# Kernel tuning notes

Measured on AMD Instinct MI355X. Metric: run time of the kernel, lower is better.

The kernel has to match this reference:

```python
import jax, jax.numpy as jnp
import numpy as np

EPS = float(np.finfo(np.float64).eps)  # np.finfo(float).eps as in the torch code
N_WAY = 64  # num_classes


def setup_inputs() -> dict:
    key = jax.random.key(0)
    k1, k2, k3, k4 = jax.random.split(key, 4)
    N, d, C, Ns = 4096, 256, N_WAY, 1024
    embeddings = jax.random.normal(k1, (N, d), dtype=jnp.float32)
    # per-node sigma from RelationNetwork; keep in [0.5, 1.5] so exp(-dist/2) is well-scaled
    sigma = jax.random.uniform(k2, (N, 1), dtype=jnp.float32, minval=0.5, maxval=1.5)
    alpha = jnp.full((1,), 0.99, dtype=jnp.float32)  # propagation coefficient
    support_labels = jax.random.randint(k3, (Ns,), 0, C)
    return {
        "embeddings": embeddings,
        "sigma": sigma,
        "alpha": alpha,
        "support_labels": support_labels,
        "alpha_k": 20,
    }


def reference(embeddings, sigma, alpha, support_labels, alpha_k):
    N, d = embeddings.shape
    C = N_WAY
    Ns = support_labels.shape[0]
    # embeddings divided by sigma twice, as in the original
    e = embeddings / (sigma + EPS)
    e = e / (sigma + EPS)
    # W_ij = mean_k (e_i - e_j)^2  via |a|^2 + |b|^2 - 2 a.b (same math, no NxNxd tensor)
    sq = jnp.sum(e * e, axis=1)  # [N]
    dist = (sq[:, None] + sq[None, :] - 2.0 * (e @ e.T)) / d  # [N, N]
    W = jnp.exp(-dist / 2.0)
    # topk per row -> scatter 1s -> symmetrize
    _, idx = jax.lax.top_k(W, alpha_k)  # [N, k]
    rows = jnp.arange(N)[:, None]
    mask = jnp.zeros_like(W).at[rows, idx].set(1.0)
    mask = ((mask + mask.T) > 0).astype(W.dtype)
    W = W * mask
    # symmetric degree normalization: S = D^-1/2 W D^-1/2
    D = W.sum(axis=0)
    d_inv_sqrt = jnp.sqrt(1.0 / (D + EPS))
    S = d_inv_sqrt[:, None] * W * d_inv_sqrt[None, :]
    # labels: one-hot support, zeros for queries
    one_hot_support = jax.nn.one_hot(support_labels, C, dtype=W.dtype)
    label_all = jnp.concatenate([one_hot_support, jnp.zeros((N - Ns, C), W.dtype)], axis=0)
    # closed-form propagation: F = (I - alpha*S + eps)^-1 @ label_all
    A = jnp.eye(N, dtype=W.dtype) - alpha[0] * S + EPS
    F = jnp.linalg.solve(A, label_all)  # same math as inverse @ labels
    return F
```

## Files before the change

### kernel.cpp

```cpp
#include <hip/hip_runtime.h>
#include <math.h>

#define NN 4096
#define DD 256
#define NCLS 64
#define EPSF 2.2204460492503131e-16f
#define NITER 36
#define KMAX 64
#define TASK 32
#define NNZ_CAP (NN * 2 * KMAX)
#define MAXTASK (NNZ_CAP / TASK)
#define LDP 40

typedef __attribute__((ext_vector_type(8))) _Float16 half8;
typedef __attribute__((ext_vector_type(4))) float f32x4;

__global__ void k_prep(const float* __restrict__ emb, const float* __restrict__ sig,
                       _Float16* __restrict__ ehi, _Float16* __restrict__ elo,
                       float* __restrict__ sq) {
  int row = blockIdx.x, t = threadIdx.x;
  float s = sig[row] + EPSF;
  float v = emb[row * DD + t];
  v = v / s; v = v / s;
  _Float16 h = (_Float16)v;
  _Float16 l = (_Float16)(v - (float)h);
  ehi[row * DD + t] = h;
  elo[row * DD + t] = l;
  __shared__ float red[DD];
  red[t] = v * v; __syncthreads();
  for (int off = 128; off > 0; off >>= 1) {
    if (t < off) red[t] += red[t + off];
    __syncthreads();
  }
  if (t == 0) sq[row] = red[0];
}

__global__ __launch_bounds__(256) void k_gemmw(
    const _Float16* __restrict__ ehi, const _Float16* __restrict__ elo,
    const float* __restrict__ sq, float* __restrict__ W) {
  __shared__ _Float16 Ah[128][LDP];
  __shared__ _Float16 Al[128][LDP];
  __shared__ _Float16 Bh[128][LDP];
  __shared__ _Float16 Bl[128][LDP];
  int t = threadIdx.x;
  int lane = t & 63, wv = t >> 6;
  int wm = wv >> 1, wn = wv & 1;
  int rowbase = blockIdx.y * 128, colbase = blockIdx.x * 128;
  f32x4 acc[4][4];
#pragma unroll
  for (int m = 0; m < 4; ++m)
#pragma unroll
    for (int n = 0; n < 4; ++n) acc[m][n] = (f32x4){0.f, 0.f, 0.f, 0.f};
  int fr = lane & 15, kc = (lane >> 4) * 8;
  for (int k0 = 0; k0 < DD; k0 += 32) {
    for (int q = t; q < 512; q += 256) {
      int lr = q >> 2, ls = (q & 3) * 8;
      size_t ga = (size_t)(rowbase + lr) * DD + k0 + ls;
      size_t gb = (size_t)(colbase + lr) * DD + k0 + ls;
      *(uint4*)&Ah[lr][ls] = *(const uint4*)&ehi[ga];
      *(uint4*)&Al[lr][ls] = *(const uint4*)&elo[ga];
      *(uint4*)&Bh[lr][ls] = *(const uint4*)&ehi[gb];
      *(uint4*)&Bl[lr][ls] = *(const uint4*)&elo[gb];
    }
    __syncthreads();
    half8 ah[4], al[4], bh[4], bl[4];
#pragma unroll
    for (int m = 0; m < 4; ++m) {
      ah[m] = *(const half8*)&Ah[wm * 64 + m * 16 + fr][kc];
      al[m] = *(const half8*)&Al[wm * 64 + m * 16 + fr][kc];
    }
#pragma unroll
    for (int n = 0; n < 4; ++n) {
      bh[n] = *(const half8*)&Bh[wn * 64 + n * 16 + fr][kc];
      bl[n] = *(const half8*)&Bl[wn * 64 + n * 16 + fr][kc];
    }
#pragma unroll
    for (int m = 0; m < 4; ++m)
#pragma unroll
      for (int n = 0; n < 4; ++n) {
        acc[m][n] = __builtin_amdgcn_mfma_f32_16x16x32_f16(ah[m], bh[n], acc[m][n], 0, 0, 0);
        acc[m][n] = __builtin_amdgcn_mfma_f32_16x16x32_f16(ah[m], bl[n], acc[m][n], 0, 0, 0);
        acc[m][n] = __builtin_amdgcn_mfma_f32_16x16x32_f16(al[m], bh[n], acc[m][n], 0, 0, 0);
      }
    __syncthreads();
  }
#pragma unroll
  for (int m = 0; m < 4; ++m) {
#pragma unroll
    for (int reg = 0; reg < 4; ++reg) {
      int i = rowbase + wm * 64 + m * 16 + (lane >> 4) * 4 + reg;
      float sqi = sq[i];
#pragma unroll
      for (int n = 0; n < 4; ++n) {
        int j = colbase + wn * 64 + n * 16 + (lane & 15);
        float dist = (sqi + sq[j] - 2.0f * acc[m][n][reg]) * (1.0f / DD);
        W[(size_t)i * NN + j] = expf(-0.5f * dist);
      }
    }
  }
}

__global__ void k_zero(unsigned* __restrict__ p, int n) {
  int i = blockIdx.x * blockDim.x + threadIdx.x;
  if (i < n) p[i] = 0u;
}

__global__ __launch_bounds__(256) void k_topk(const float* __restrict__ W,
                                              unsigned* __restrict__ mask,
                                              const int* __restrict__ kptr) {
  int row = blockIdx.x;
  int t = threadIdx.x, lane = t & 63, w = t >> 6;
  int K = kptr[0]; if (K > KMAX) K = KMAX;
  const float* Wr = &W[(size_t)row * NN];
  float val[16];
#pragma unroll
  for (int i = 0; i < 16; ++i) val[i] = Wr[w * 1024 + i * 64 + lane];
  unsigned rm = 0;
  __shared__ float lv[4][KMAX];
  __shared__ int   lc[4][KMAX];
  for (int k = 0; k < K; ++k) {
    float vb = -1e38f; int cb = 0x7fffffff;
#pragma unroll
    for (int i = 0; i < 16; ++i) {
      bool ok = !((rm >> i) & 1u);
      if (ok && val[i] > vb) { vb = val[i]; cb = w * 1024 + i * 64 + lane; }
    }
    for (int off = 32; off > 0; off >>= 1) {
      float ov = __shfl_xor(vb, off, 64);
      int   oc = __shfl_xor(cb, off, 64);
      if (ov > vb || (ov == vb && oc < cb)) { vb = ov; cb = oc; }
    }
    if ((cb & 63) == lane) { int i = (cb >> 6) & 15; rm |= 1u << i; }
    if (lane == 0) { lv[w][k] = vb; lc[w][k] = cb; }
  }
  __syncthreads();
  if (w == 0) {
    float cv[4]; int cc[4]; unsigned crm = 0;
#pragma unroll
    for (int j = 0; j < 4; ++j) {
      if (lane < K) { cv[j] = lv[j][lane]; cc[j] = lc[j][lane]; }
      else { cv[j] = -1e38f; cc[j] = 0x7fffffff; }
    }
    for (int k = 0; k < K; ++k) {
      float vb = -1e38f; int cb = 0x7fffffff;
#pragma unroll
      for (int j = 0; j < 4; ++j) {
        bool ok = !((crm >> j) & 1u);
        if (ok && (cv[j] > vb || (cv[j] == vb && cc[j] < cb))) { vb = cv[j]; cb = cc[j]; }
      }
      for (int off = 32; off > 0; off >>= 1) {
        float ov = __shfl_xor(vb, off, 64);
        int   oc = __shfl_xor(cb, off, 64);
        if (ov > vb || (ov == vb && oc < cb)) { vb = ov; cb = oc; }
      }
#pragma unroll
      for (int j = 0; j < 4; ++j) if (cc[j] == cb) crm |= 1u << j;
      if (lane == 0) {
        atomicOr(&mask[row * 128 + (cb >> 5)], 1u << (cb & 31));
        atomicOr(&mask[cb * 128 + (row >> 5)], 1u << (row & 31));
      }
    }
  }
}

__global__ void k_degree(const unsigned* __restrict__ mask, const float* __restrict__ W,
                         float* __restrict__ Dinv, int* __restrict__ deg) {
  int row = blockIdx.x, t = threadIdx.x;
  unsigned m = mask[row * 128 + t];
  float dsum = 0.f; int cnt = __popc(m);
  unsigned mm = m;
  while (mm) {
    int b = __ffs(mm) - 1; mm &= mm - 1;
    dsum += W[(size_t)row * NN + t * 32 + b];
  }
  __shared__ float rs[128];
  __shared__ int   rc[128];
  rs[t] = dsum; rc[t] = cnt; __syncthreads();
  for (int off = 64; off > 0; off >>= 1) {
    if (t < off) { rs[t] += rs[t + off]; rc[t] += rc[t + off]; }
    __syncthreads();
  }
  if (t == 0) { deg[row] = rc[0]; Dinv[row] = sqrtf(1.0f / (rs[0] + EPSF)); }
}

__global__ void k_scan(const int* __restrict__ deg, int* __restrict__ rowptr) {
  int t = threadIdx.x;
  int lane = t & 63, w = t >> 6;
  int loc[16]; int s = 0;
  for (int u = 0; u < 16; ++u) { loc[u] = s; s += deg[t * 16 + u]; }
  int tot = s, inc = s;
  for (int off = 1; off < 64; off <<= 1) {
    int n = __shfl_up(inc, off, 64);
    if (lane >= off) inc += n;
  }
  __shared__ int wt[4];
  if (lane == 63) wt[w] = inc;
  __syncthreads();
  int base = 0;
  for (int u = 0; u < w; ++u) base += wt[u];
  int excl = base + inc - tot;
  for (int u = 0; u < 16; ++u) rowptr[t * 16 + u] = excl + loc[u];
  if (t == 255) rowptr[NN] = excl + tot;
}

__global__ void k_fill(const unsigned* __restrict__ mask, const float* __restrict__ W,
                       const float* __restrict__ Dinv, const int* __restrict__ rowptr,
                       int2* __restrict__ cv, const float* __restrict__ alphap) {
  int row = blockIdx.x, t = threadIdx.x;
  float alpha = alphap[0];
  unsigned m = mask[row * 128 + t];
  __shared__ int wcnt[128];
  wcnt[t] = __popc(m); __syncthreads();
  int pre = 0;
  for (int u = 0; u < t; ++u) pre += wcnt[u];
  int base = rowptr[row] + pre;
  float di = Dinv[row];
  while (m) {
    int b = __ffs(m) - 1; m &= m - 1;
    int j = t * 32 + b;
    float v = alpha * W[(size_t)row * NN + j] * di * Dinv[j];
    cv[base] = make_int2(j, __float_as_int(v));
    ++base;
  }
}

__global__ void k_taskrow(const int* __restrict__ rowptr, int* __restrict__ taskrow) {
  int task = blockIdx.x * blockDim.x + threadIdx.x;
  int nnz = rowptr[NN];
  int ntask = (nnz + TASK - 1) / TASK;
  if (task >= ntask) return;
  int start = task * TASK;
  int lo = 0, hi = NN;
  while (hi - lo > 1) {
    int mid = (lo + hi) >> 1;
    if (rowptr[mid] <= start) lo = mid; else hi = mid;
  }
  taskrow[task] = lo;
}

__global__ __launch_bounds__(256) void k_init_state(
    const int* __restrict__ labels, int Ns, float* __restrict__ X,
    float* __restrict__ R, float* __restrict__ D0, float* __restrict__ SV) {
  int idx = blockIdx.x * 256 + threadIdx.x;
  int i = idx >> 6, c = idx & 63;
  float b = (i < Ns && labels[i] == c) ? 1.0f : 0.0f;
  X[idx] = 0.0f; R[idx] = b; D0[idx] = b; SV[idx] = 0.0f;
}

__global__ __launch_bounds__(256) void k_spmm(
    const int* __restrict__ rowptr, const int2* __restrict__ cv,
    const int* __restrict__ taskrow, const float* __restrict__ Dc,
    float* __restrict__ SV) {
  int lane = threadIdx.x & 63;
  int wave0 = (blockIdx.x * 256 + threadIdx.x) >> 6;
  int nwaves = (gridDim.x * 256) >> 6;
  int nnz = rowptr[NN];
  int ntask = (nnz + TASK - 1) / TASK;
  for (int task = wave0; task < ntask; task += nwaves) {
    int start = task * TASK;
    int end = start + TASK; if (end > nnz) end = nnz;
    float prod[TASK];
#pragma unroll
    for (int u = 0; u < TASK; ++u) {
      int p = start + u;
      if (p < end) {
        int2 c = cv[p];
        prod[u] = __int_as_float(c.y) * Dc[(size_t)c.x * 64 + lane];
      } else prod[u] = 0.0f;
    }
    int r = taskrow[task];
    int rend = rowptr[r + 1];
    float acc = 0.0f;
#pragma unroll
    for (int u = 0; u < TASK; ++u) {
      int p = start + u;
      if (p >= end) break;
      while (p >= rend) {
        atomicAdd(&SV[(size_t)r * 64 + lane], acc);
        acc = 0.0f; ++r; rend = rowptr[r + 1];
      }
      acc += prod[u];
    }
    atomicAdd(&SV[(size_t)r * 64 + lane], acc);
  }
}

__global__ __launch_bounds__(256) void k_update(
    float* __restrict__ X, float* __restrict__ R, const float* __restrict__ Dcur,
    float* __restrict__ Dnxt, float* __restrict__ SV,
    const float* __restrict__ alphap, int it) {
  int idx = (blockIdx.x * 256 + threadIdx.x) * 2;
  float alpha = alphap[0];
  float sigma1 = 1.0f / alpha;
  float rho_prev = alpha;
  for (int k = 0; k < it; ++k) rho_prev = 1.0f / (2.0f * sigma1 - rho_prev);
  float rho = 1.0f / (2.0f * sigma1 - rho_prev);
  float c1 = rho * rho_prev, c2 = 2.0f * rho / alpha;
  float2 s = *(float2*)&SV[idx];
  *(float2*)&SV[idx] = make_float2(0.f, 0.f);
  float2 d = *(const float2*)&Dcur[idx];
  float2 x = *(float2*)&X[idx];
  float2 r = *(float2*)&R[idx];
  x.x += d.x; x.y += d.y;
  r.x -= (d.x - s.x); r.y -= (d.y - s.y);
  float2 dn;
  dn.x = c1 * d.x + c2 * r.x; dn.y = c1 * d.y + c2 * r.y;
  *(float2*)&X[idx] = x;
  *(float2*)&R[idx] = r;
  *(float2*)&Dnxt[idx] = dn;
}

static inline char* carve(char*& p, size_t bytes) {
  char* r = p;
  size_t a = (bytes + 255) & ~(size_t)255;
  p += a;
  return r;
}

extern "C" void kernel_launch(void* const* d_in, const int* in_sizes, int n_in,
                              void* d_out, int out_size, void* d_ws, size_t ws_size,
                              hipStream_t stream) {
  const float* emb    = (const float*)d_in[0];
  const float* sigma  = (const float*)d_in[1];
  const float* alphap = (const float*)d_in[2];
  const int*   labels = (const int*)d_in[3];
  const int*   kptr   = (const int*)d_in[4];
  int Ns = in_sizes[3];
  float* X = (float*)d_out;

  char* p = (char*)d_ws;
  _Float16* ehi    = (_Float16*)carve(p, (size_t)NN * DD * 2);
  _Float16* elo    = (_Float16*)carve(p, (size_t)NN * DD * 2);
  float*    sq     = (float*)carve(p, NN * 4);
  float*    Wm     = (float*)carve(p, (size_t)NN * NN * 4);
  unsigned* mask   = (unsigned*)carve(p, NN * 128 * 4);
  float*    Dinv   = (float*)carve(p, NN * 4);
  int*      deg    = (int*)carve(p, NN * 4);
  int*      rowptr = (int*)carve(p, (NN + 1) * 4);
  int2*     cv     = (int2*)carve(p, (size_t)NNZ_CAP * 8);
  int*      trow   = (int*)carve(p, (size_t)MAXTASK * 4);
  float*    Rbuf   = (float*)carve(p, (size_t)NN * NCLS * 4);
  float*    SV     = (float*)carve(p, (size_t)NN * NCLS * 4);
  float*    Db0    = (float*)carve(p, (size_t)NN * NCLS * 4);
  float*    Db1    = (float*)carve(p, (size_t)NN * NCLS * 4);

  k_prep<<<NN, DD, 0, stream>>>(emb, sigma, ehi, elo, sq);
  k_gemmw<<<dim3(NN / 128, NN / 128), 256, 0, stream>>>(ehi, elo, sq, Wm);
  k_zero<<<(NN * 128 + 255) / 256, 256, 0, stream>>>(mask, NN * 128);
  k_topk<<<NN, 256, 0, stream>>>(Wm, mask, kptr);
  k_degree<<<NN, 128, 0, stream>>>(mask, Wm, Dinv, deg);
  k_scan<<<1, 256, 0, stream>>>(deg, rowptr);
  k_fill<<<NN, 128, 0, stream>>>(mask, Wm, Dinv, rowptr, cv, alphap);
  k_taskrow<<<(MAXTASK + 255) / 256, 256, 0, stream>>>(rowptr, trow);

  k_init_state<<<(NN * NCLS) / 256, 256, 0, stream>>>(labels, Ns, X, Rbuf, Db0, SV);
  for (int it = 0; it < NITER; ++it) {
    float* Dc = (it & 1) ? Db1 : Db0;
    float* Dn = (it & 1) ? Db0 : Db1;
    k_spmm<<<1280, 256, 0, stream>>>(rowptr, cv, trow, Dc, SV);
    k_update<<<(NN * NCLS) / 512, 256, 0, stream>>>(X, Rbuf, Dc, Dn, SV, alphap, it);
  }
}
```

Measured before the change: 1.078 ms.

## Use radix-histogram threshold to prefilter top-k candidates per row

The top-k kernel now stages each row in shared memory and builds a 2048-bin histogram on the high bits of the float values. From that it finds the threshold bin holding the K-th largest value and gathers only the elements at or above it into a small candidate list. The iterative max-selection then runs over at most 1024 candidates instead of all 4096 values per wave. A serial single-wave fallback covers rows whose candidate count overflows, and the change adds about 25KB of shared memory per block, which may lower occupancy.

```diff
diff --git a/kernel.cpp b/kernel.cpp
--- a/kernel.cpp
+++ b/kernel.cpp
@@ -11,6 +11,7 @@
 #define NNZ_CAP (NN * 2 * KMAX)
 #define MAXTASK (NNZ_CAP / TASK)
 #define LDP 40
+#define CAND_CAP 1024
 
 typedef __attribute__((ext_vector_type(8))) _Float16 half8;
 typedef __attribute__((ext_vector_type(4))) float f32x4;
@@ -111,42 +112,72 @@
   int row = blockIdx.x;
   int t = threadIdx.x, lane = t & 63, w = t >> 6;
   int K = kptr[0]; if (K > KMAX) K = KMAX;
-  const float* Wr = &W[(size_t)row * NN];
-  float val[16];
-#pragma unroll
-  for (int i = 0; i < 16; ++i) val[i] = Wr[w * 1024 + i * 64 + lane];
-  unsigned rm = 0;
+  __shared__ float rowv[NN];
+  __shared__ int   hist[2048];
+  __shared__ int   candi[CAND_CAP];
   __shared__ float lv[4][KMAX];
   __shared__ int   lc[4][KMAX];
-  for (int k = 0; k < K; ++k) {
-    float vb = -1e38f; int cb = 0x7fffffff;
-#pragma unroll
-    for (int i = 0; i < 16; ++i) {
-      bool ok = !((rm >> i) & 1u);
-      if (ok && val[i] > vb) { vb = val[i]; cb = w * 1024 + i * 64 + lane; }
-    }
-    for (int off = 32; off > 0; off >>= 1) {
-      float ov = __shfl_xor(vb, off, 64);
-      int   oc = __shfl_xor(cb, off, 64);
-      if (ov > vb || (ov == vb && oc < cb)) { vb = ov; cb = oc; }
-    }
-    if ((cb & 63) == lane) { int i = (cb >> 6) & 15; rm |= 1u << i; }
-    if (lane == 0) { lv[w][k] = vb; lc[w][k] = cb; }
-  }
-  __syncthreads();
-  if (w == 0) {
-    float cv[4]; int cc[4]; unsigned crm = 0;
-#pragma unroll
-    for (int j = 0; j < 4; ++j) {
-      if (lane < K) { cv[j] = lv[j][lane]; cc[j] = lc[j][lane]; }
-      else { cv[j] = -1e38f; cc[j] = 0x7fffffff; }
-    }
+  __shared__ int   wt[4];
+  __shared__ int   thr_bin, cand_cnt;
+  const float* Wr = &W[(size_t)row * NN];
+  for (int b = t; b < 2048; b += 256) hist[b] = 0;
+  if (t == 0) cand_cnt = 0;
+  __syncthreads();
+  for (int j4 = t; j4 < NN / 4; j4 += 256) {
+    float4 f = ((const float4*)Wr)[j4];
+    *(float4*)&rowv[j4 * 4] = f;
+    atomicAdd(&hist[__float_as_uint(f.x) >> 21], 1);
+    atomicAdd(&hist[__float_as_uint(f.y) >> 21], 1);
+    atomicAdd(&hist[__float_as_uint(f.z) >> 21], 1);
+    atomicAdd(&hist[__float_as_uint(f.w) >> 21], 1);
+  }
+  __syncthreads();
+  int loc[8]; int s = 0;
+#pragma unroll
+  for (int u = 0; u < 8; ++u) { loc[u] = hist[t * 8 + u]; s += loc[u]; }
+  int inc = s;
+  for (int off = 1; off < 64; off <<= 1) {
+    int n = __shfl_up(inc, off, 64);
+    if (lane >= off) inc += n;
+  }
+  if (lane == 63) wt[w] = inc;
+  __syncthreads();
+  int base = 0;
+  for (int u = 0; u < w; ++u) base += wt[u];
+  int Pincl = base + inc;
+  int above = NN - Pincl;
+  if (above < K && K <= above + s) {
+    int cum = above;
+    for (int u = 7; u >= 0; --u) {
+      cum += loc[u];
+      if (cum >= K) { thr_bin = t * 8 + u; break; }
+    }
+  }
+  __syncthreads();
+  int tb = thr_bin;
+  for (int j = t; j < NN; j += 256) {
+    if ((int)(__float_as_uint(rowv[j]) >> 21) >= tb) {
+      int p = atomicAdd(&cand_cnt, 1);
+      if (p < CAND_CAP) candi[p] = j;
+    }
+  }
+  __syncthreads();
+  int C = cand_cnt;
+  if (C <= CAND_CAP) {
+    float cv[4]; int ci[4];
+#pragma unroll
+    for (int q = 0; q < 4; ++q) {
+      int p = w * 256 + q * 64 + lane;
+      if (p < C) { ci[q] = candi[p]; cv[q] = rowv[ci[q]]; }
+      else { cv[q] = -1e38f; ci[q] = 0x7fffffff; }
+    }
+    unsigned rm = 0;
     for (int k = 0; k < K; ++k) {
       float vb = -1e38f; int cb = 0x7fffffff;
 #pragma unroll
-      for (int j = 0; j < 4; ++j) {
-        bool ok = !((crm >> j) & 1u);
-        if (ok && (cv[j] > vb || (cv[j] == vb && cc[j] < cb))) { vb = cv[j]; cb = cc[j]; }
+      for (int q = 0; q < 4; ++q) {
+        bool ok = !((rm >> q) & 1u);
+        if (ok && (cv[q] > vb || (cv[q] == vb && ci[q] < cb))) { vb = cv[q]; cb = ci[q]; }
       }
       for (int off = 32; off > 0; off >>= 1) {
         float ov = __shfl_xor(vb, off, 64);
@@ -154,7 +185,50 @@
         if (ov > vb || (ov == vb && oc < cb)) { vb = ov; cb = oc; }
       }
 #pragma unroll
-      for (int j = 0; j < 4; ++j) if (cc[j] == cb) crm |= 1u << j;
+      for (int q = 0; q < 4; ++q) if (ci[q] == cb) rm |= 1u << q;
+      if (lane == 0) { lv[w][k] = vb; lc[w][k] = cb; }
+    }
+    __syncthreads();
+    if (w == 0) {
+      float mv[4]; int mc[4]; unsigned crm = 0;
+#pragma unroll
+      for (int j = 0; j < 4; ++j) {
+        if (lane < K) { mv[j] = lv[j][lane]; mc[j] = lc[j][lane]; }
+        else { mv[j] = -1e38f; mc[j] = 0x7fffffff; }
+      }
+      for (int k = 0; k < K; ++k) {
+        float vb = -1e38f; int cb = 0x7fffffff;
+#pragma unroll
+        for (int j = 0; j < 4; ++j) {
+          bool ok = !((crm >> j) & 1u);
+          if (ok && (mv[j] > vb || (mv[j] == vb && mc[j] < cb))) { vb = mv[j]; cb = mc[j]; }
+        }
+        for (int off = 32; off > 0; off >>= 1) {
+          float ov = __shfl_xor(vb, off, 64);
+          int   oc = __shfl_xor(cb, off, 64);
+          if (ov > vb || (ov == vb && oc < cb)) { vb = ov; cb = oc; }
+        }
+#pragma unroll
+        for (int j = 0; j < 4; ++j) if (mc[j] == cb) crm |= 1u << j;
+        if (lane == 0) {
+          atomicOr(&mask[row * 128 + (cb >> 5)], 1u << (cb & 31));
+          atomicOr(&mask[cb * 128 + (row >> 5)], 1u << (row & 31));
+        }
+      }
+    }
+  } else if (w == 0) {
+    for (int k = 0; k < K; ++k) {
+      float vb = -1e38f; int cb = 0x7fffffff;
+      for (int i = 0; i < 64; ++i) {
+        float v = rowv[i * 64 + lane];
+        if (v > vb) { vb = v; cb = i * 64 + lane; }
+      }
+      for (int off = 32; off > 0; off >>= 1) {
+        float ov = __shfl_xor(vb, off, 64);
+        int   oc = __shfl_xor(cb, off, 64);
+        if (ov > vb || (ov == vb && oc < cb)) { vb = ov; cb = oc; }
+      }
+      if ((cb & 63) == lane) rowv[cb] = -1e38f;
       if (lane == 0) {
         atomicOr(&mask[row * 128 + (cb >> 5)], 1u << (cb & 31));
         atomicOr(&mask[cb * 128 + (row >> 5)], 1u << (row & 31));
```

Measured after the change: 1.133 ms. 1.05x slower.
